# Optimization experiments

Hardware: AMD Instinct MI355X
Metric: run time of the kernel (lower is better)

Reference implementation:

```python
import jax, jax.numpy as jnp
import numpy as np

K = 2  # max_diffusion_step
UNITS = 128
NUM_NODES = 1024


def _diffusion_conv(x, support, W, b):
    # x: (B, N, D) ; Chebyshev diffusion over scaled Laplacian support (N, N)
    x0 = x
    x1 = jnp.einsum('nm,bmd->bnd', support, x0)
    xs = [x0, x1]
    for _ in range(K - 1):
        xs.append(2.0 * jnp.einsum('nm,bmd->bnd', support, xs[-1]) - xs[-2])
    feats = jnp.concatenate(xs, axis=-1)  # (B, N, D*(K+1))
    return feats @ W + b


def _gclstm_cell(x, h, c, support, W, b):
    gates = _diffusion_conv(jnp.concatenate([x, h], axis=-1), support, W, b)
    i, f, o, g = jnp.split(gates, 4, axis=-1)
    c_new = jax.nn.sigmoid(f) * c + jax.nn.sigmoid(i) * jnp.tanh(g)
    h_new = jax.nn.sigmoid(o) * jnp.tanh(c_new)
    return h_new, c_new


def setup_inputs() -> dict:
    key = jax.random.key(0)
    ks = jax.random.split(key, 8)
    B, S, N, H = 64, 12, NUM_NODES, UNITS

    # build scaled-Laplacian support from a sparse random symmetric adjacency
    rng = np.random.default_rng(0)
    A = (rng.random((N, N)) < 0.01).astype(np.float32)
    A = np.maximum(A, A.T)
    np.fill_diagonal(A, 0.0)
    d = A.sum(axis=1)
    d_is = 1.0 / np.sqrt(np.maximum(d, 1.0))
    L = np.eye(N, dtype=np.float32) - (d_is[:, None] * A * d_is[None, :])
    support = (L - np.eye(N, dtype=np.float32)).astype(np.float32)  # lambda_max ~ 2

    def lin(k, shape, fan_in):
        return jax.random.normal(k, shape, jnp.float32) / np.sqrt(fan_in)

    return {
        'inputs': jax.random.normal(ks[0], (B, N, 1), jnp.float32),
        'encoder_outputs': jax.random.normal(ks[1], (S, B, N, H), jnp.float32),
        'hidden_state': jax.random.normal(ks[2], (2, B, N, H), jnp.float32),
        'cell_state': jax.random.normal(ks[3], (2, B, N, H), jnp.float32),
        'supports': jnp.asarray(support),
        'w0': lin(ks[4], ((1 + H) * (K + 1), 4 * H), (1 + H) * (K + 1)),
        'b0': jnp.zeros((4 * H,), jnp.float32),
        'w1': lin(ks[5], ((H + H) * (K + 1), 4 * H), 2 * H * (K + 1)),
        'b1': jnp.zeros((4 * H,), jnp.float32),
        'attn_w': lin(ks[6], (H, H), H),
        'attn_b': jnp.zeros((H,), jnp.float32),
        'proj_w': lin(ks[7], (2 * H, 1), 2 * H),
        'proj_b': jnp.zeros((1,), jnp.float32),
    }


def reference(inputs, encoder_outputs, hidden_state, cell_state, supports,
              w0, b0, w1, b1, attn_w, attn_b, proj_w, proj_b):
    out = inputs
    hs, cs = [], []
    for layer, (W, b) in enumerate([(w0, b0), (w1, b1)]):
        h_new, c_new = _gclstm_cell(out, hidden_state[layer], cell_state[layer],
                                    supports, W, b)
        hs.append(h_new)
        cs.append(c_new)
        out = h_new  # (B, N, H)

    # additive attention: energy (S,B,N) -> softmax over S
    energy = jnp.tanh(encoder_outputs @ attn_w + attn_b)          # (S,B,N,H)
    energy = jnp.sum(energy * out[None], axis=-1)                 # (S,B,N)
    attention_weights = jax.nn.softmax(jnp.transpose(energy, (1, 2, 0)), axis=-1)  # (B,N,S)

    # bmm context gather
    context = jnp.einsum('bns,sbnh->bnh', attention_weights, encoder_outputs)

    cat = jnp.concatenate([out, context], axis=-1)                # (B,N,2H)
    projected = cat @ proj_w + proj_b                             # (B,N,out_dim)
    B = out.shape[0]
    output = projected.reshape(B, -1)                             # (B, N*out_dim)
    return output, jnp.stack(hs), jnp.stack(cs), attention_weights
```

## Files before the change

kernel.cpp:

```cpp
#include <hip/hip_runtime.h>
#include <hip/hip_bf16.h>
#include <stdint.h>

#define NB 64
#define NN 1024
#define NH 128
#define NS 12
#define BN (NB*NN)
#define D0 129
#define K0P 416
#define K1 768
#define NG 512
#define MAXNNZ 128

typedef __hip_bfloat16 bf16;
typedef float v4f __attribute__((ext_vector_type(4)));
typedef __bf16 v8bf __attribute__((ext_vector_type(8)));

__device__ __forceinline__ float bf2f(bf16 x) { return __bfloat162float(x); }
__device__ __forceinline__ bf16 f2bf(float x) { return __float2bfloat16(x); }
__device__ __forceinline__ float sane(float x) { return __builtin_isfinite(x) ? x : 0.f; }
__device__ __forceinline__ float sigf(float x) { return 1.f / (1.f + __expf(-x)); }
__device__ __forceinline__ float tanhfast(float x) { return 1.f - 2.f / (1.f + __expf(2.f * x)); }

__device__ __forceinline__ float loadF(const void* p, size_t i, int f32) {
  return f32 ? ((const float*)p)[i] : bf2f(((const bf16*)p)[i]);
}
__device__ __forceinline__ void storeF(void* p, size_t i, float v, int f32) {
  if (f32) ((float*)p)[i] = v; else ((bf16*)p)[i] = f2bf(v);
}
__device__ __forceinline__ v8bf load8(const void* p, size_t i, int f32) {
  if (f32) {
    const float4 a = *(const float4*)((const float*)p + i);
    const float4 b = *(const float4*)((const float*)p + i + 4);
    union { v8bf v; __hip_bfloat162 h[4]; } u;
    u.h[0] = __float22bfloat162_rn(make_float2(a.x, a.y));
    u.h[1] = __float22bfloat162_rn(make_float2(a.z, a.w));
    u.h[2] = __float22bfloat162_rn(make_float2(b.x, b.y));
    u.h[3] = __float22bfloat162_rn(make_float2(b.z, b.w));
    return u.v;
  }
  return *(const v8bf*)((const bf16*)p + i);
}

__global__ void detect_dtype(const unsigned short* __restrict__ probe, int* __restrict__ flag) {
  int t = threadIdx.x;
  unsigned short x = probe[2 * t];
  int e = (x >> 7) & 0xFF;
  int insane = !((x & 0x7FFF) == 0 || (e >= 117 && e <= 131));
  __shared__ int cnt;
  if (t == 0) cnt = 0;
  __syncthreads();
  atomicAdd(&cnt, insane);
  __syncthreads();
  if (t == 0) *flag = (cnt > 64) ? 1 : 0;
}

__global__ void build_csr(const void* __restrict__ sup, int* __restrict__ cols,
                          float* __restrict__ vals, int* __restrict__ cnt,
                          const int* __restrict__ flag) {
  int f32 = *flag;
  int n = blockIdx.x;
  __shared__ int cn;
  if (threadIdx.x == 0) cn = 0;
  __syncthreads();
  for (int m = threadIdx.x; m < NN; m += blockDim.x) {
    float v = loadF(sup, (size_t)n * NN + m, f32);
    if (v != 0.0f && __builtin_isfinite(v)) {
      int slot = atomicAdd(&cn, 1);
      if (slot < MAXNNZ) { cols[n * MAXNNZ + slot] = m; vals[n * MAXNNZ + slot] = v; }
    }
  }
  __syncthreads();
  if (threadIdx.x == 0) cnt[n] = (cn < MAXNNZ) ? cn : MAXNNZ;
}

__global__ void pack_wt(const void* __restrict__ w, bf16* __restrict__ bt,
                        int K, int Kp, int Nn, const int* __restrict__ flag) {
  int f32 = *flag;
  int n = blockIdx.x;
  for (int k = threadIdx.x; k < Kp; k += blockDim.x) {
    float v = (k < K) ? loadF(w, (size_t)k * Nn + n, f32) : 0.0f;
    bt[(size_t)n * Kp + k] = f2bf(v);
  }
}

__global__ void diffuse0_a(const void* __restrict__ xin, const void* __restrict__ h0,
                           const int* __restrict__ cols, const float* __restrict__ vals,
                           const int* __restrict__ cnt, bf16* __restrict__ feats,
                           const int* __restrict__ flag) {
  int f32 = *flag;
  int bn = blockIdx.x;
  int n = bn & (NN - 1);
  int b = bn >> 10;
  int d = threadIdx.x;
  bf16* frow = feats + (size_t)bn * K0P;
  if (d < D0) {
    float x0 = (d == 0) ? loadF(xin, bn, f32) : loadF(h0, (size_t)bn * NH + d - 1, f32);
    frow[d] = f2bf(x0);
    float acc = 0.f;
    int c = cnt[n];
    for (int j = 0; j < c; ++j) {
      int m = cols[n * MAXNNZ + j];
      float s = vals[n * MAXNNZ + j];
      int bm = (b << 10) | m;
      float xv = (d == 0) ? loadF(xin, bm, f32) : loadF(h0, (size_t)bm * NH + d - 1, f32);
      acc += s * xv;
    }
    frow[D0 + d] = f2bf(acc);
  } else if (d < D0 + (K0P - 3 * D0)) {
    frow[3 * D0 + (d - D0)] = f2bf(0.f);
  }
}

__global__ void diffuse0_b(const void* __restrict__ xin, const void* __restrict__ h0,
                           const int* __restrict__ cols, const float* __restrict__ vals,
                           const int* __restrict__ cnt, bf16* __restrict__ feats,
                           const int* __restrict__ flag) {
  int f32 = *flag;
  int bn = blockIdx.x;
  int n = bn & (NN - 1);
  int b = bn >> 10;
  int d = threadIdx.x;
  if (d >= D0) return;
  float x0 = (d == 0) ? loadF(xin, bn, f32) : loadF(h0, (size_t)bn * NH + d - 1, f32);
  float acc = -x0;
  int c = cnt[n];
  for (int j = 0; j < c; ++j) {
    int m = cols[n * MAXNNZ + j];
    float s = vals[n * MAXNNZ + j];
    int bm = (b << 10) | m;
    float x1 = bf2f(feats[(size_t)bm * K0P + D0 + d]);
    acc += 2.f * s * x1;
  }
  feats[(size_t)bn * K0P + 2 * D0 + d] = f2bf(acc);
}

__global__ void diffuse1_a(const void* __restrict__ dout, size_t offH0,
                           const void* __restrict__ hidden, size_t offH1in,
                           const int* __restrict__ cols, const float* __restrict__ vals,
                           const int* __restrict__ cnt, bf16* __restrict__ feats,
                           const int* __restrict__ flag) {
  int f32 = *flag;
  int bn = blockIdx.x;
  int n = bn & (NN - 1);
  int b = bn >> 10;
  int d = threadIdx.x;
  bf16* frow = feats + (size_t)bn * K1;
  float x0 = (d < NH) ? loadF(dout, offH0 + (size_t)bn * NH + d, f32)
                      : loadF(hidden, offH1in + (size_t)bn * NH + d - NH, f32);
  frow[d] = f2bf(x0);
  float acc = 0.f;
  int c = cnt[n];
  for (int j = 0; j < c; ++j) {
    int m = cols[n * MAXNNZ + j];
    float s = vals[n * MAXNNZ + j];
    size_t bm = (size_t)((b << 10) | m) * NH;
    float xv = (d < NH) ? loadF(dout, offH0 + bm + d, f32)
                        : loadF(hidden, offH1in + bm + d - NH, f32);
    acc += s * xv;
  }
  frow[256 + d] = f2bf(acc);
}

__global__ void diffuse1_b(const void* __restrict__ dout, size_t offH0,
                           const void* __restrict__ hidden, size_t offH1in,
                           const int* __restrict__ cols, const float* __restrict__ vals,
                           const int* __restrict__ cnt, bf16* __restrict__ feats,
                           const int* __restrict__ flag) {
  int f32 = *flag;
  int bn = blockIdx.x;
  int n = bn & (NN - 1);
  int b = bn >> 10;
  int d = threadIdx.x;
  float x0 = (d < NH) ? loadF(dout, offH0 + (size_t)bn * NH + d, f32)
                      : loadF(hidden, offH1in + (size_t)bn * NH + d - NH, f32);
  float acc = -x0;
  int c = cnt[n];
  for (int j = 0; j < c; ++j) {
    int m = cols[n * MAXNNZ + j];
    float s = vals[n * MAXNNZ + j];
    int bm = (b << 10) | m;
    float x1 = bf2f(feats[(size_t)bm * K1 + 256 + d]);
    acc += 2.f * s * x1;
  }
  feats[(size_t)bn * K1 + 512 + d] = f2bf(acc);
}

__global__ __launch_bounds__(256) void gemm_bt(const bf16* __restrict__ A,
    const bf16* __restrict__ Bt, const void* __restrict__ bias,
    bf16* __restrict__ C, int Kd, const int* __restrict__ flag) {
  int f32 = *flag;
  __shared__ __align__(16) unsigned short As[128 * 32];
  __shared__ __align__(16) unsigned short Bs[128 * 32];
  const int tid = threadIdx.x;
  const int l = tid & 63;
  const int w = tid >> 6;
  const int wm = w >> 1, wn = w & 1;
  const int m0 = blockIdx.x * 128;
  const int n0 = blockIdx.y * 128;
  const bf16* Ab = A + (size_t)m0 * Kd;
  const bf16* Bb = Bt + (size_t)n0 * Kd;
  const int lr = l & 15, q = l >> 4;
  v4f acc[4][4] = {};
  for (int k0 = 0; k0 < Kd; k0 += 32) {
    v8bf ga[2], gb[2];
#pragma unroll
    for (int t = 0; t < 2; ++t) {
      int s = tid + 256 * t;
      int row = s >> 2, col = (s & 3) * 8;
      ga[t] = *(const v8bf*)(Ab + (size_t)row * Kd + k0 + col);
      gb[t] = *(const v8bf*)(Bb + (size_t)row * Kd + k0 + col);
    }
    __syncthreads();
#pragma unroll
    for (int t = 0; t < 2; ++t) {
      int s = tid + 256 * t;
      int row = s >> 2, col = (s & 3) * 8;
      *(v8bf*)&As[row * 32 + col] = ga[t];
      *(v8bf*)&Bs[row * 32 + col] = gb[t];
    }
    __syncthreads();
    v8bf af[4], bfv[4];
#pragma unroll
    for (int i = 0; i < 4; ++i) {
      af[i]  = *(const v8bf*)&As[(wm * 64 + i * 16 + lr) * 32 + q * 8];
      bfv[i] = *(const v8bf*)&Bs[(wn * 64 + i * 16 + lr) * 32 + q * 8];
    }
#pragma unroll
    for (int mt = 0; mt < 4; ++mt)
#pragma unroll
      for (int nt = 0; nt < 4; ++nt)
        acc[mt][nt] = __builtin_amdgcn_mfma_f32_16x16x32_bf16(af[mt], bfv[nt], acc[mt][nt], 0, 0, 0);
    __syncthreads();
  }
#pragma unroll
  for (int nt = 0; nt < 4; ++nt) {
    int n = n0 + wn * 64 + nt * 16 + lr;
    float bv = loadF(bias, n, f32);
#pragma unroll
    for (int mt = 0; mt < 4; ++mt)
#pragma unroll
      for (int r = 0; r < 4; ++r) {
        int m = m0 + wm * 64 + mt * 16 + q * 4 + r;
        C[(size_t)m * NG + n] = f2bf(acc[mt][nt][r] + bv);
      }
  }
}

__global__ __launch_bounds__(128) void lstm_cell(const bf16* __restrict__ gates,
    const void* __restrict__ cell, size_t offCin, void* __restrict__ dout,
    size_t offH, size_t offC, const int* __restrict__ flag) {
  int f32 = *flag;
  size_t bn = blockIdx.x;
  int h = threadIdx.x;
  const bf16* g = gates + bn * NG;
  float iv = sane(bf2f(g[h]));
  float fv = sane(bf2f(g[NH + h]));
  float ov = sane(bf2f(g[2 * NH + h]));
  float gv = sane(bf2f(g[3 * NH + h]));
  float c = sane(loadF(cell, offCin + bn * NH + h, f32));
  float cn = sigf(fv) * c + sigf(iv) * tanhfast(gv);
  float hn = sigf(ov) * tanhfast(cn);
  storeF(dout, offC + bn * NH + h, cn, f32);
  storeF(dout, offH + bn * NH + h, hn, f32);
}

#define AROWS 8
#define EPADF 132
__global__ __launch_bounds__(512) void fused_attn(const void* __restrict__ enc,
    const bf16* __restrict__ BtW, const void* __restrict__ ab,
    void* __restrict__ dout, size_t offH1, size_t offAttn,
    const void* __restrict__ pw, const void* __restrict__ pb,
    const int* __restrict__ flag) {
  int f32 = *flag;
  __shared__ __align__(16) float encsf[(NS * AROWS + 8) * EPADF];
  __shared__ float h1s[AROWS][NH];
  __shared__ float ered[NS][8][AROWS];
  __shared__ float wts[NS][AROWS];
  const int tid = threadIdx.x;
  const int l = tid & 63, w = tid >> 6;
  const int bn0 = blockIdx.x * AROWS;

  for (int i = tid; i < 8 * EPADF; i += 512) encsf[NS * AROWS * EPADF + i] = 0.f;
  for (int g = tid; g < NS * AROWS * (NH / 4); g += 512) {
    int s = g >> 8;
    int r = (g >> 5) & 7;
    int cg = g & 31;
    float4 v;
    if (f32) {
      v = *(const float4*)((const float*)enc + ((size_t)s * BN + bn0 + r) * NH + cg * 4);
    } else {
      const bf16* p = (const bf16*)enc + ((size_t)s * BN + bn0 + r) * NH + cg * 4;
      v = make_float4(bf2f(p[0]), bf2f(p[1]), bf2f(p[2]), bf2f(p[3]));
    }
    *(float4*)&encsf[(s * AROWS + r) * EPADF + cg * 4] = v;
  }
  for (int i = tid; i < AROWS * NH; i += 512) {
    int r = i >> 7, h = i & 127;
    h1s[r][h] = loadF(dout, offH1 + (size_t)(bn0 + r) * NH + h, f32);
  }
  __syncthreads();

  const int lr = l & 15, q = l >> 4;
  const int n = w * 16 + lr;
  const float bvs = loadF(ab, n, f32);
  for (int s = 0; s < NS; ++s) {
    v4f acc = {};
#pragma unroll
    for (int kk = 0; kk < 4; ++kk) {
      const float* ap = &encsf[(s * AROWS + lr) * EPADF + kk * 32 + q * 8];
      float4 a0 = *(const float4*)ap;
      float4 a1 = *(const float4*)(ap + 4);
      union { v8bf v; __hip_bfloat162 h[4]; } ua;
      ua.h[0] = __float22bfloat162_rn(make_float2(a0.x, a0.y));
      ua.h[1] = __float22bfloat162_rn(make_float2(a0.z, a0.w));
      ua.h[2] = __float22bfloat162_rn(make_float2(a1.x, a1.y));
      ua.h[3] = __float22bfloat162_rn(make_float2(a1.z, a1.w));
      v8bf bv = *(const v8bf*)(BtW + (size_t)n * NH + kk * 32 + q * 8);
      acc = __builtin_amdgcn_mfma_f32_16x16x32_bf16(ua.v, bv, acc, 0, 0, 0);
    }
    float parts[4];
#pragma unroll
    for (int r = 0; r < 4; ++r) {
      int m = q * 4 + r;
      float t = tanhfast(acc[r] + bvs);
      parts[r] = (m < AROWS) ? t * h1s[m][n] : 0.f;
    }
#pragma unroll
    for (int r = 0; r < 4; ++r) {
      float v = parts[r];
      v += __shfl_xor(v, 1);
      v += __shfl_xor(v, 2);
      v += __shfl_xor(v, 4);
      v += __shfl_xor(v, 8);
      int m = q * 4 + r;
      if (lr == 0 && m < AROWS) ered[s][w][m] = v;
    }
  }
  __syncthreads();
  if (tid < AROWS) {
    int m = tid;
    float e[NS];
    float mx = -3.4e38f;
#pragma unroll
    for (int s = 0; s < NS; ++s) {
      float v = 0.f;
#pragma unroll
      for (int ww = 0; ww < 8; ++ww) v += ered[s][ww][m];
      e[s] = sane(v);
      mx = fmaxf(mx, e[s]);
    }
    float sum = 0.f;
#pragma unroll
    for (int s = 0; s < NS; ++s) { e[s] = __expf(e[s] - mx); sum += e[s]; }
    float inv = 1.f / sum;
#pragma unroll
    for (int s = 0; s < NS; ++s) wts[s][m] = e[s] * inv;
  }
  __syncthreads();
  if (tid < AROWS * NS) {
    int m = tid / NS, s = tid - m * NS;
    storeF(dout, offAttn + (size_t)(bn0 + m) * NS + s, wts[s][m], f32);
  }
  {
    int m = w;
    float part = 0.f;
#pragma unroll
    for (int hh = 0; hh < 2; ++hh) {
      int h = l + hh * 64;
      float ctx = 0.f;
#pragma unroll
      for (int s = 0; s < NS; ++s)
        ctx += wts[s][m] * encsf[(s * AROWS + m) * EPADF + h];
      part += sane(h1s[m][h] * loadF(pw, h, f32) + ctx * loadF(pw, NH + h, f32));
    }
#pragma unroll
    for (int mask = 1; mask < 64; mask <<= 1) part += __shfl_xor(part, mask);
    if (l == 0) storeF(dout, bn0 + m, part + loadF(pb, 0, f32), f32);
  }
}

extern "C" void kernel_launch(void* const* d_in, const int* in_sizes, int n_in,
                              void* d_out, int out_size, void* d_ws, size_t ws_size,
                              hipStream_t stream) {
  const void* xin    = d_in[0];
  const void* enc    = d_in[1];
  const void* hidden = d_in[2];
  const void* cell   = d_in[3];
  const void* sup    = d_in[4];
  const void* w0     = d_in[5];
  const void* b0     = d_in[6];
  const void* w1     = d_in[7];
  const void* b1     = d_in[8];
  const void* aw     = d_in[9];
  const void* ab     = d_in[10];
  const void* pw     = d_in[11];
  const void* pb     = d_in[12];

  char* ws = (char*)d_ws;
  size_t off = 0;
  auto alloc = [&](size_t bytes) -> char* {
    char* p = ws + off;
    off += (bytes + 255) & ~(size_t)255;
    return p;
  };
  bf16*  feats    = (bf16*)alloc((size_t)BN * K1 * 2);
  bf16*  gates    = (bf16*)alloc((size_t)BN * NG * 2);
  bf16*  Bt0      = (bf16*)alloc((size_t)NG * K0P * 2);
  bf16*  Bt1      = (bf16*)alloc((size_t)NG * K1 * 2);
  bf16*  BtA      = (bf16*)alloc((size_t)NH * NH * 2);
  int*   csr_cols = (int*)alloc((size_t)NN * MAXNNZ * 4);
  float* csr_vals = (float*)alloc((size_t)NN * MAXNNZ * 4);
  int*   csr_cnt  = (int*)alloc((size_t)NN * 4);
  int*   flag     = (int*)alloc(256);

  const size_t OFF_HS   = (size_t)BN;
  const size_t OFF_CS   = OFF_HS + (size_t)2 * BN * NH;
  const size_t OFF_ATTN = OFF_CS + (size_t)2 * BN * NH;
  const size_t OFF_H0 = OFF_HS;
  const size_t OFF_H1 = OFF_HS + (size_t)BN * NH;
  const size_t OFF_C0 = OFF_CS;
  const size_t OFF_C1 = OFF_CS + (size_t)BN * NH;
  const size_t LAYER1 = (size_t)BN * NH;

  detect_dtype<<<1, 256, 0, stream>>>((const unsigned short*)cell, flag);
  build_csr<<<NN, 256, 0, stream>>>(sup, csr_cols, csr_vals, csr_cnt, flag);
  pack_wt<<<NG, 256, 0, stream>>>(w0, Bt0, 387, K0P, NG, flag);
  pack_wt<<<NG, 256, 0, stream>>>(w1, Bt1, K1, K1, NG, flag);
  pack_wt<<<NH, 128, 0, stream>>>(aw, BtA, NH, NH, NH, flag);

  diffuse0_a<<<BN, 192, 0, stream>>>(xin, hidden, csr_cols, csr_vals, csr_cnt, feats, flag);
  diffuse0_b<<<BN, 192, 0, stream>>>(xin, hidden, csr_cols, csr_vals, csr_cnt, feats, flag);
  {
    dim3 g(BN / 128, NG / 128);
    gemm_bt<<<g, 256, 0, stream>>>(feats, Bt0, b0, gates, K0P, flag);
  }
  lstm_cell<<<BN, 128, 0, stream>>>(gates, cell, 0, d_out, OFF_H0, OFF_C0, flag);

  diffuse1_a<<<BN, 256, 0, stream>>>(d_out, OFF_H0, hidden, LAYER1,
                                     csr_cols, csr_vals, csr_cnt, feats, flag);
  diffuse1_b<<<BN, 256, 0, stream>>>(d_out, OFF_H0, hidden, LAYER1,
                                     csr_cols, csr_vals, csr_cnt, feats, flag);
  {
    dim3 g(BN / 128, NG / 128);
    gemm_bt<<<g, 256, 0, stream>>>(feats, Bt1, b1, gates, K1, flag);
  }
  lstm_cell<<<BN, 128, 0, stream>>>(gates, cell, LAYER1, d_out, OFF_H1, OFF_C1, flag);

  fused_attn<<<BN / AROWS, 512, 0, stream>>>(enc, BtA, ab, d_out, OFF_H1, OFF_ATTN,
                                             pw, pb, flag);
}
```

Baseline: 2.110 ms.

## Rewrite attention as 128-row tiled kernel with online softmax context accumulation

Replaces the 8-row-per-block attention kernel with a 128-row tile per block. Each block stages the attention weight matrix once in shared memory as bf16 and streams encoder tiles per timestep through MFMA. An online (flash-style) softmax accumulates the context in registers, so all 12 encoder timesteps no longer have to be held at once. This cuts per-block weight reloads and wastes fewer MFMA rows (the old 16-row tiles had 8 rows masked). In exchange it adds per-timestep barriers, reads h1 from global repeatedly, and computes the context from bf16-rounded encoder values, which lowers precision.

Result: faster. 1.901 ms (-9.9%).

```diff
diff --git a/kernel.cpp b/kernel.cpp
--- a/kernel.cpp
+++ b/kernel.cpp
@@ -266,118 +266,134 @@
   storeF(dout, offH + bn * NH + h, hn, f32);
 }
 
-#define AROWS 8
-#define EPADF 132
-__global__ __launch_bounds__(512) void fused_attn(const void* __restrict__ enc,
+#define FPAD 132
+__global__ __launch_bounds__(512, 4) void flash_attn(const void* __restrict__ enc,
     const bf16* __restrict__ BtW, const void* __restrict__ ab,
     void* __restrict__ dout, size_t offH1, size_t offAttn,
     const void* __restrict__ pw, const void* __restrict__ pb,
     const int* __restrict__ flag) {
   int f32 = *flag;
-  __shared__ __align__(16) float encsf[(NS * AROWS + 8) * EPADF];
-  __shared__ float h1s[AROWS][NH];
-  __shared__ float ered[NS][8][AROWS];
-  __shared__ float wts[NS][AROWS];
+  __shared__ __align__(16) unsigned short Ws[128 * FPAD];
+  __shared__ __align__(16) unsigned short Es[128 * FPAD];
+  __shared__ float ered[4][128];
+  __shared__ float eall[NS][128];
+  __shared__ float mxs[128], sms[128], psl[128], all[128];
   const int tid = threadIdx.x;
   const int l = tid & 63, w = tid >> 6;
-  const int bn0 = blockIdx.x * AROWS;
-
-  for (int i = tid; i < 8 * EPADF; i += 512) encsf[NS * AROWS * EPADF + i] = 0.f;
-  for (int g = tid; g < NS * AROWS * (NH / 4); g += 512) {
-    int s = g >> 8;
-    int r = (g >> 5) & 7;
-    int cg = g & 31;
-    float4 v;
-    if (f32) {
-      v = *(const float4*)((const float*)enc + ((size_t)s * BN + bn0 + r) * NH + cg * 4);
-    } else {
-      const bf16* p = (const bf16*)enc + ((size_t)s * BN + bn0 + r) * NH + cg * 4;
-      v = make_float4(bf2f(p[0]), bf2f(p[1]), bf2f(p[2]), bf2f(p[3]));
-    }
-    *(float4*)&encsf[(s * AROWS + r) * EPADF + cg * 4] = v;
-  }
-  for (int i = tid; i < AROWS * NH; i += 512) {
-    int r = i >> 7, h = i & 127;
-    h1s[r][h] = loadF(dout, offH1 + (size_t)(bn0 + r) * NH + h, f32);
-  }
-  __syncthreads();
-
+  const int wm = w >> 2, wn = w & 3;
   const int lr = l & 15, q = l >> 4;
-  const int n = w * 16 + lr;
-  const float bvs = loadF(ab, n, f32);
+  const int bn0 = blockIdx.x * 128;
+
+  for (int i = tid; i < 128 * 16; i += 512) {
+    int row = i >> 4, c = i & 15;
+    *(v8bf*)&Ws[row * FPAD + c * 8] = *(const v8bf*)(BtW + (size_t)row * NH + c * 8);
+  }
+  if (tid < 128) { mxs[tid] = -3.4e38f; sms[tid] = 0.f; }
+
+  float ctx[32];
+#pragma unroll
+  for (int j = 0; j < 32; ++j) ctx[j] = 0.f;
+  const int cm = tid >> 2;
+  const int ch0 = (tid & 3) * 32;
+
+  float abv[2];
+#pragma unroll
+  for (int nt = 0; nt < 2; ++nt) abv[nt] = loadF(ab, wn * 32 + nt * 16 + lr, f32);
+
   for (int s = 0; s < NS; ++s) {
-    v4f acc = {};
-#pragma unroll
-    for (int kk = 0; kk < 4; ++kk) {
-      const float* ap = &encsf[(s * AROWS + lr) * EPADF + kk * 32 + q * 8];
-      float4 a0 = *(const float4*)ap;
-      float4 a1 = *(const float4*)(ap + 4);
-      union { v8bf v; __hip_bfloat162 h[4]; } ua;
-      ua.h[0] = __float22bfloat162_rn(make_float2(a0.x, a0.y));
-      ua.h[1] = __float22bfloat162_rn(make_float2(a0.z, a0.w));
-      ua.h[2] = __float22bfloat162_rn(make_float2(a1.x, a1.y));
-      ua.h[3] = __float22bfloat162_rn(make_float2(a1.z, a1.w));
-      v8bf bv = *(const v8bf*)(BtW + (size_t)n * NH + kk * 32 + q * 8);
-      acc = __builtin_amdgcn_mfma_f32_16x16x32_bf16(ua.v, bv, acc, 0, 0, 0);
-    }
-    float parts[4];
-#pragma unroll
-    for (int r = 0; r < 4; ++r) {
-      int m = q * 4 + r;
-      float t = tanhfast(acc[r] + bvs);
-      parts[r] = (m < AROWS) ? t * h1s[m][n] : 0.f;
-    }
-#pragma unroll
-    for (int r = 0; r < 4; ++r) {
-      float v = parts[r];
-      v += __shfl_xor(v, 1);
-      v += __shfl_xor(v, 2);
-      v += __shfl_xor(v, 4);
-      v += __shfl_xor(v, 8);
-      int m = q * 4 + r;
-      if (lr == 0 && m < AROWS) ered[s][w][m] = v;
-    }
-  }
-  __syncthreads();
-  if (tid < AROWS) {
-    int m = tid;
-    float e[NS];
-    float mx = -3.4e38f;
+    __syncthreads();
+#pragma unroll
+    for (int t = 0; t < 4; ++t) {
+      int idx = tid + 512 * t;
+      int row = idx >> 4, c = idx & 15;
+      *(v8bf*)&Es[row * FPAD + c * 8] = load8(enc, ((size_t)s * BN + bn0 + row) * NH + c * 8, f32);
+    }
+    __syncthreads();
+    v4f acc[4][2] = {};
+    for (int k0 = 0; k0 < NH; k0 += 32) {
+      v8bf af[4], bv[2];
+#pragma unroll
+      for (int mt = 0; mt < 4; ++mt)
+        af[mt] = *(const v8bf*)&Es[(wm * 64 + mt * 16 + lr) * FPAD + k0 + q * 8];
+#pragma unroll
+      for (int nt = 0; nt < 2; ++nt)
+        bv[nt] = *(const v8bf*)&Ws[(wn * 32 + nt * 16 + lr) * FPAD + k0 + q * 8];
+#pragma unroll
+      for (int mt = 0; mt < 4; ++mt)
+#pragma unroll
+        for (int nt = 0; nt < 2; ++nt)
+          acc[mt][nt] = __builtin_amdgcn_mfma_f32_16x16x32_bf16(af[mt], bv[nt], acc[mt][nt], 0, 0, 0);
+    }
+#pragma unroll
+    for (int mt = 0; mt < 4; ++mt) {
+      float parts[4] = {0.f, 0.f, 0.f, 0.f};
+#pragma unroll
+      for (int nt = 0; nt < 2; ++nt) {
+        int n = wn * 32 + nt * 16 + lr;
+#pragma unroll
+        for (int r = 0; r < 4; ++r) {
+          int m = wm * 64 + mt * 16 + q * 4 + r;
+          float t = tanhfast(acc[mt][nt][r] + abv[nt]);
+          parts[r] += t * loadF(dout, offH1 + (size_t)(bn0 + m) * NH + n, f32);
+        }
+      }
+#pragma unroll
+      for (int r = 0; r < 4; ++r) {
+        float v = parts[r];
+        v += __shfl_xor(v, 1);
+        v += __shfl_xor(v, 2);
+        v += __shfl_xor(v, 4);
+        v += __shfl_xor(v, 8);
+        if (lr == 0) ered[wn][wm * 64 + mt * 16 + q * 4 + r] = v;
+      }
+    }
+    __syncthreads();
+    if (tid < 128) {
+      float e = sane(ered[0][tid] + ered[1][tid] + ered[2][tid] + ered[3][tid]);
+      eall[s][tid] = e;
+      float mo = mxs[tid];
+      float mn = fmaxf(mo, e);
+      float a = __expf(mo - mn);
+      float p = __expf(e - mn);
+      sms[tid] = sms[tid] * a + p;
+      mxs[tid] = mn;
+      all[tid] = a;
+      psl[tid] = p;
+    }
+    __syncthreads();
+    {
+      float a = all[cm], p = psl[cm];
+      const unsigned short* ep = &Es[cm * FPAD + ch0];
+#pragma unroll
+      for (int j = 0; j < 32; ++j)
+        ctx[j] = ctx[j] * a + p * __uint_as_float((unsigned)ep[j] << 16);
+    }
+  }
+  __syncthreads();
+  if (tid < 128) {
+    float inv = 1.f / sms[tid];
+    all[tid] = inv;
+    float mxf = mxs[tid];
 #pragma unroll
     for (int s = 0; s < NS; ++s) {
-      float v = 0.f;
-#pragma unroll
-      for (int ww = 0; ww < 8; ++ww) v += ered[s][ww][m];
-      e[s] = sane(v);
-      mx = fmaxf(mx, e[s]);
-    }
-    float sum = 0.f;
-#pragma unroll
-    for (int s = 0; s < NS; ++s) { e[s] = __expf(e[s] - mx); sum += e[s]; }
-    float inv = 1.f / sum;
-#pragma unroll
-    for (int s = 0; s < NS; ++s) wts[s][m] = e[s] * inv;
-  }
-  __syncthreads();
-  if (tid < AROWS * NS) {
-    int m = tid / NS, s = tid - m * NS;
-    storeF(dout, offAttn + (size_t)(bn0 + m) * NS + s, wts[s][m], f32);
-  }
+      float wv = __expf(eall[s][tid] - mxf) * inv;
+      storeF(dout, offAttn + (size_t)(bn0 + tid) * NS + s, wv, f32);
+    }
+  }
+  __syncthreads();
   {
-    int m = w;
+    float inv = all[cm];
     float part = 0.f;
 #pragma unroll
-    for (int hh = 0; hh < 2; ++hh) {
-      int h = l + hh * 64;
-      float ctx = 0.f;
-#pragma unroll
-      for (int s = 0; s < NS; ++s)
-        ctx += wts[s][m] * encsf[(s * AROWS + m) * EPADF + h];
-      part += sane(h1s[m][h] * loadF(pw, h, f32) + ctx * loadF(pw, NH + h, f32));
-    }
-#pragma unroll
-    for (int mask = 1; mask < 64; mask <<= 1) part += __shfl_xor(part, mask);
-    if (l == 0) storeF(dout, bn0 + m, part + loadF(pb, 0, f32), f32);
+    for (int j = 0; j < 32; ++j) {
+      int h = ch0 + j;
+      float hv = loadF(dout, offH1 + (size_t)(bn0 + cm) * NH + h, f32);
+      part += hv * loadF(pw, h, f32) + ctx[j] * inv * loadF(pw, NH + h, f32);
+    }
+    part = sane(part);
+    part += __shfl_xor(part, 1);
+    part += __shfl_xor(part, 2);
+    if ((tid & 3) == 0) storeF(dout, bn0 + cm, part + loadF(pb, 0, f32), f32);
   }
 }
 
@@ -448,6 +464,6 @@
   }
   lstm_cell<<<BN, 128, 0, stream>>>(gates, cell, LAYER1, d_out, OFF_H1, OFF_C1, flag);
 
-  fused_attn<<<BN / AROWS, 512, 0, stream>>>(enc, BtA, ab, d_out, OFF_H1, OFF_ATTN,
-                                             pw, pb, flag);
-}
+  flash_attn<<<BN / 128, 512, 0, stream>>>(enc, BtA, ab, d_out, OFF_H1, OFF_ATTN,
+                                           pw, pb, flag);
+}
```
